# Kernel optimization log

Measured on AMD Instinct MI355X. Metric: run time of the kernel, lower is better.

## Reference

```python
import jax, jax.numpy as jnp
import numpy as np

T = 8192
D_IN = 512
D_QK = 64
D_V = 64


def setup_inputs() -> dict:
    key = jax.random.key(0)
    kx, kq, kk, kv, kl = jax.random.split(key, 5)
    x = jax.random.normal(kx, (T, D_IN), dtype=jnp.float32)
    Wq = jax.random.normal(kq, (D_IN, D_QK), dtype=jnp.float32) * 0.02
    Wk = jax.random.normal(kk, (D_IN, D_QK), dtype=jnp.float32) * 0.02
    Wv = jax.random.normal(kv, (D_IN, D_V), dtype=jnp.float32) * 0.02
    l = jax.random.normal(kl, (T, T), dtype=jnp.float32) * 0.02
    return {"x": x, "Wq": Wq, "Wk": Wk, "Wv": Wv, "l": l}


def reference(x, Wq, Wk, Wv, l):
    # q: [T, d_qk], k: [T, d_qk], v: [T, d_v]
    q = x @ Wq
    k = x @ Wk
    v = x @ Wv
    # scores: [T, S] = (q k^T) elementwise-weighted by learned tril matrix
    scores = jnp.einsum("tn,sn->ts", q, k) * jnp.tril(l)
    # output: [T, d_v]
    return scores @ v
```

## Files before the change

kernel.cpp:

```cpp
#include <hip/hip_runtime.h>
#include <hip/hip_bf16.h>

#define TT 8192
#define DIN 512
#define DQK 64

typedef __attribute__((ext_vector_type(8))) short short8;
typedef __attribute__((ext_vector_type(4))) float f32x4;

__global__ __launch_bounds__(256) void zero_kernel(float* __restrict__ out, int n4)
{
    int i = blockIdx.x * 256 + threadIdx.x;
    if (i < n4) ((f32x4*)out)[i] = (f32x4){0.f, 0.f, 0.f, 0.f};
}

#define PP 72

__global__ __launch_bounds__(256) void proj_kernel(
    const float* __restrict__ x,
    const float* __restrict__ Wq, const float* __restrict__ Wk, const float* __restrict__ Wv,
    __hip_bfloat16* __restrict__ qb, __hip_bfloat16* __restrict__ kb,
    __hip_bfloat16* __restrict__ vt)
{
    __shared__ short xb[64][PP];
    __shared__ short wb[3][64][PP];

    const int rowBase = blockIdx.x * 64;
    const int tid = threadIdx.x;
    const int lane = tid & 63;
    const int w = tid >> 6;
    const int lo = lane & 15, hi = lane >> 4;

    f32x4 acc[3][4];
    #pragma unroll
    for (int m = 0; m < 3; ++m)
        #pragma unroll
        for (int cf = 0; cf < 4; ++cf) acc[m][cf] = (f32x4){0.f, 0.f, 0.f, 0.f};

    for (int kk = 0; kk < DIN; kk += 64) {
        {
            const int r = tid >> 2;
            const int c0 = (tid & 3) * 16;
            const float* xp = x + (size_t)(rowBase + r) * DIN + kk + c0;
            short tmp[16];
            #pragma unroll
            for (int j = 0; j < 16; ++j) {
                __hip_bfloat16 h = __float2bfloat16(xp[j]);
                tmp[j] = *(short*)&h;
            }
            *(short8*)&xb[r][c0]     = *(short8*)&tmp[0];
            *(short8*)&xb[r][c0 + 8] = *(short8*)&tmp[8];
        }
        {
            const int kr = tid >> 2;
            const int c0 = (tid & 3) * 16;
            #pragma unroll
            for (int m = 0; m < 3; ++m) {
                const float* Wm = (m == 0 ? Wq : (m == 1 ? Wk : Wv));
                const float* wp = Wm + (size_t)(kk + kr) * DQK + c0;
                #pragma unroll
                for (int j = 0; j < 16; ++j) {
                    __hip_bfloat16 h = __float2bfloat16(wp[j]);
                    wb[m][c0 + j][kr] = *(short*)&h;
                }
            }
        }
        __syncthreads();

        short8 a0 = *(short8*)&xb[w * 16 + lo][hi * 8];
        short8 a1 = *(short8*)&xb[w * 16 + lo][32 + hi * 8];
        #pragma unroll
        for (int m = 0; m < 3; ++m) {
            #pragma unroll
            for (int cf = 0; cf < 4; ++cf) {
                short8 b0 = *(short8*)&wb[m][cf * 16 + lo][hi * 8];
                short8 b1 = *(short8*)&wb[m][cf * 16 + lo][32 + hi * 8];
                acc[m][cf] = __builtin_amdgcn_mfma_f32_16x16x32_bf16(a0, b0, acc[m][cf], 0, 0, 0);
                acc[m][cf] = __builtin_amdgcn_mfma_f32_16x16x32_bf16(a1, b1, acc[m][cf], 0, 0, 0);
            }
        }
        __syncthreads();
    }

    #pragma unroll
    for (int cf = 0; cf < 4; ++cf) {
        #pragma unroll
        for (int r = 0; r < 4; ++r) {
            const int tg = rowBase + w * 16 + hi * 4 + r;
            const int d  = cf * 16 + lo;
            __hip_bfloat16 hq = __float2bfloat16(acc[0][cf][r]);
            __hip_bfloat16 hk = __float2bfloat16(acc[1][cf][r]);
            __hip_bfloat16 hv = __float2bfloat16(acc[2][cf][r]);
            qb[(size_t)tg * DQK + d] = hq;
            kb[(size_t)tg * DQK + d] = hk;
            vt[(size_t)d * TT + tg]  = hv;
        }
    }
}

#define TM 128
#define TS 64
#define SCHUNK 256
#define LP 72

__global__ __launch_bounds__(512) void attn_kernel(
    const __hip_bfloat16* __restrict__ qb,
    const __hip_bfloat16* __restrict__ kb,
    const __hip_bfloat16* __restrict__ vt,
    const float* __restrict__ l,
    float* __restrict__ out)
{
    __shared__ short K_lds[TS][LP];
    __shared__ short V_lds[DQK][LP];
    __shared__ short S_lds[8][16][LP];

    const int t0 = blockIdx.x * TM;
    const int sStart = blockIdx.y * SCHUNK;
    if (sStart >= t0 + TM) return;
    const int sEnd = min(sStart + SCHUNK, t0 + TM);

    const int tid = threadIdx.x;
    const int lane = tid & 63;
    const int w = tid >> 6;
    const int lo = lane & 15, hi = lane >> 4;
    const int trow = t0 + w * 16;

    short8 qf0, qf1;
    {
        const short* qp = (const short*)qb + (size_t)(trow + lo) * DQK;
        qf0 = *(const short8*)(qp + hi * 8);
        qf1 = *(const short8*)(qp + 32 + hi * 8);
    }

    f32x4 acc_o[4];
    #pragma unroll
    for (int i = 0; i < 4; ++i) acc_o[i] = (f32x4){0.f, 0.f, 0.f, 0.f};

    for (int s0 = sStart; s0 < sEnd; s0 += TS) {
        {
            const int row = tid >> 3;
            const int c8 = (tid & 7) * 8;
            *(short8*)&K_lds[row][c8] =
                *(const short8*)((const short*)kb + (size_t)(s0 + row) * DQK + c8);
            *(short8*)&V_lds[row][c8] =
                *(const short8*)((const short*)vt + (size_t)row * TT + s0 + c8);
        }
        __syncthreads();

        const bool active = (s0 <= trow + 15);

        if (active) {
            float lv[4][4];
            #pragma unroll
            for (int sub = 0; sub < 4; ++sub) {
                const int s_glob = s0 + sub * 16 + lo;
                #pragma unroll
                for (int r = 0; r < 4; ++r) {
                    const int tg = trow + hi * 4 + r;
                    lv[sub][r] = (s_glob <= tg) ? l[(size_t)tg * TT + s_glob] : 0.f;
                }
            }
            #pragma unroll
            for (int sub = 0; sub < 4; ++sub) {
                f32x4 acc = (f32x4){0.f, 0.f, 0.f, 0.f};
                short8 b0 = *(short8*)&K_lds[sub * 16 + lo][hi * 8];
                short8 b1 = *(short8*)&K_lds[sub * 16 + lo][32 + hi * 8];
                acc = __builtin_amdgcn_mfma_f32_16x16x32_bf16(qf0, b0, acc, 0, 0, 0);
                acc = __builtin_amdgcn_mfma_f32_16x16x32_bf16(qf1, b1, acc, 0, 0, 0);
                #pragma unroll
                for (int r = 0; r < 4; ++r) {
                    float sv = acc[r] * lv[sub][r];
                    __hip_bfloat16 h = __float2bfloat16(sv);
                    S_lds[w][hi * 4 + r][sub * 16 + lo] = *(short*)&h;
                }
            }
        }
        __syncthreads();

        if (active) {
            short8 a0 = *(short8*)&S_lds[w][lo][hi * 8];
            short8 a1 = *(short8*)&S_lds[w][lo][32 + hi * 8];
            #pragma unroll
            for (int ds = 0; ds < 4; ++ds) {
                short8 b0 = *(short8*)&V_lds[ds * 16 + lo][hi * 8];
                short8 b1 = *(short8*)&V_lds[ds * 16 + lo][32 + hi * 8];
                acc_o[ds] = __builtin_amdgcn_mfma_f32_16x16x32_bf16(a0, b0, acc_o[ds], 0, 0, 0);
                acc_o[ds] = __builtin_amdgcn_mfma_f32_16x16x32_bf16(a1, b1, acc_o[ds], 0, 0, 0);
            }
        }
        __syncthreads();
    }

    #pragma unroll
    for (int ds = 0; ds < 4; ++ds) {
        #pragma unroll
        for (int r = 0; r < 4; ++r) {
            const int tg = trow + hi * 4 + r;
            atomicAdd(&out[(size_t)tg * DQK + ds * 16 + lo], acc_o[ds][r]);
        }
    }
}

extern "C" void kernel_launch(void* const* d_in, const int* in_sizes, int n_in,
                              void* d_out, int out_size, void* d_ws, size_t ws_size,
                              hipStream_t stream) {
    const float* x  = (const float*)d_in[0];
    const float* Wq = (const float*)d_in[1];
    const float* Wk = (const float*)d_in[2];
    const float* Wv = (const float*)d_in[3];
    const float* l  = (const float*)d_in[4];
    float* out = (float*)d_out;

    __hip_bfloat16* qb = (__hip_bfloat16*)d_ws;
    __hip_bfloat16* kb = qb + (size_t)TT * DQK;
    __hip_bfloat16* vt = kb + (size_t)TT * DQK;

    zero_kernel<<<(out_size / 4 + 255) / 256, 256, 0, stream>>>(out, out_size / 4);
    proj_kernel<<<TT / 64, 256, 0, stream>>>(x, Wq, Wk, Wv, qb, kb, vt);
    attn_kernel<<<dim3(TT / TM, TT / SCHUNK), 512, 0, stream>>>(qb, kb, vt, l, out);
}
```

Measured before the change: 77.82 us.

## Prefetch next l tile in registers, pre-convert weights, vectorize x loads

```diff
diff --git a/kernel.cpp b/kernel.cpp
--- a/kernel.cpp
+++ b/kernel.cpp
@@ -14,11 +14,47 @@
     if (i < n4) ((f32x4*)out)[i] = (f32x4){0.f, 0.f, 0.f, 0.f};
 }
 
+__global__ __launch_bounds__(256) void wconv_kernel(
+    const float* __restrict__ Wq, const float* __restrict__ Wk, const float* __restrict__ Wv,
+    __hip_bfloat16* __restrict__ wtb)
+{
+    __shared__ float tile[64][65];
+    const int m = blockIdx.y;
+    const float* W = m == 0 ? Wq : (m == 1 ? Wk : Wv);
+    const int k0 = blockIdx.x * 64;
+    const int tid = threadIdx.x;
+
+    {
+        const int col4 = (tid & 15) * 4;
+        #pragma unroll
+        for (int it = 0; it < 4; ++it) {
+            const int row = (tid >> 4) + it * 16;
+            float4 v = *(const float4*)&W[(size_t)(k0 + row) * DQK + col4];
+            tile[row][col4 + 0] = v.x; tile[row][col4 + 1] = v.y;
+            tile[row][col4 + 2] = v.z; tile[row][col4 + 3] = v.w;
+        }
+    }
+    __syncthreads();
+    {
+        const int d = tid >> 2;
+        const int kc = (tid & 3) * 16;
+        short tmp[16];
+        #pragma unroll
+        for (int j = 0; j < 16; ++j) {
+            __hip_bfloat16 h = __float2bfloat16(tile[kc + j][d]);
+            tmp[j] = *(short*)&h;
+        }
+        short* dst = (short*)wtb + ((size_t)m * 64 + d) * DIN + k0 + kc;
+        *(short8*)dst       = *(short8*)&tmp[0];
+        *(short8*)(dst + 8) = *(short8*)&tmp[8];
+    }
+}
+
 #define PP 72
 
 __global__ __launch_bounds__(256) void proj_kernel(
     const float* __restrict__ x,
-    const float* __restrict__ Wq, const float* __restrict__ Wk, const float* __restrict__ Wv,
+    const __hip_bfloat16* __restrict__ wtb,
     __hip_bfloat16* __restrict__ qb, __hip_bfloat16* __restrict__ kb,
     __hip_bfloat16* __restrict__ vt)
 {
@@ -44,25 +80,26 @@
             const float* xp = x + (size_t)(rowBase + r) * DIN + kk + c0;
             short tmp[16];
             #pragma unroll
-            for (int j = 0; j < 16; ++j) {
-                __hip_bfloat16 h = __float2bfloat16(xp[j]);
-                tmp[j] = *(short*)&h;
+            for (int j = 0; j < 16; j += 4) {
+                float4 v = *(const float4*)(xp + j);
+                __hip_bfloat16 h0 = __float2bfloat16(v.x);
+                __hip_bfloat16 h1 = __float2bfloat16(v.y);
+                __hip_bfloat16 h2 = __float2bfloat16(v.z);
+                __hip_bfloat16 h3 = __float2bfloat16(v.w);
+                tmp[j + 0] = *(short*)&h0; tmp[j + 1] = *(short*)&h1;
+                tmp[j + 2] = *(short*)&h2; tmp[j + 3] = *(short*)&h3;
             }
             *(short8*)&xb[r][c0]     = *(short8*)&tmp[0];
             *(short8*)&xb[r][c0 + 8] = *(short8*)&tmp[8];
         }
         {
-            const int kr = tid >> 2;
-            const int c0 = (tid & 3) * 16;
+            const int d = tid >> 2;
+            const int kc = (tid & 3) * 16;
             #pragma unroll
             for (int m = 0; m < 3; ++m) {
-                const float* Wm = (m == 0 ? Wq : (m == 1 ? Wk : Wv));
-                const float* wp = Wm + (size_t)(kk + kr) * DQK + c0;
-                #pragma unroll
-                for (int j = 0; j < 16; ++j) {
-                    __hip_bfloat16 h = __float2bfloat16(wp[j]);
-                    wb[m][c0 + j][kr] = *(short*)&h;
-                }
+                const short* src = (const short*)wtb + ((size_t)m * 64 + d) * DIN + kk + kc;
+                *(short8*)&wb[m][d][kc]     = *(const short8*)src;
+                *(short8*)&wb[m][d][kc + 8] = *(const short8*)(src + 8);
             }
         }
         __syncthreads();
@@ -136,6 +173,20 @@
     #pragma unroll
     for (int i = 0; i < 4; ++i) acc_o[i] = (f32x4){0.f, 0.f, 0.f, 0.f};
 
+    float lvC[4][4];
+    float lvN[4][4] = {{0.f}};
+    {
+        #pragma unroll
+        for (int sub = 0; sub < 4; ++sub) {
+            const int s_glob = sStart + sub * 16 + lo;
+            #pragma unroll
+            for (int r = 0; r < 4; ++r) {
+                const int tg = trow + hi * 4 + r;
+                lvC[sub][r] = (s_glob <= tg) ? l[(size_t)tg * TT + s_glob] : 0.f;
+            }
+        }
+    }
+
     for (int s0 = sStart; s0 < sEnd; s0 += TS) {
         {
             const int row = tid >> 3;
@@ -148,18 +199,22 @@
         __syncthreads();
 
         const bool active = (s0 <= trow + 15);
-
-        if (active) {
-            float lv[4][4];
+        const int sN = s0 + TS;
+        const bool act_next = (sN < sEnd) && (sN <= trow + 15);
+
+        if (act_next) {
             #pragma unroll
             for (int sub = 0; sub < 4; ++sub) {
-                const int s_glob = s0 + sub * 16 + lo;
+                const int s_glob = sN + sub * 16 + lo;
                 #pragma unroll
                 for (int r = 0; r < 4; ++r) {
                     const int tg = trow + hi * 4 + r;
-                    lv[sub][r] = (s_glob <= tg) ? l[(size_t)tg * TT + s_glob] : 0.f;
+                    lvN[sub][r] = (s_glob <= tg) ? l[(size_t)tg * TT + s_glob] : 0.f;
                 }
             }
+        }
+
+        if (active) {
             #pragma unroll
             for (int sub = 0; sub < 4; ++sub) {
                 f32x4 acc = (f32x4){0.f, 0.f, 0.f, 0.f};
@@ -169,15 +224,11 @@
                 acc = __builtin_amdgcn_mfma_f32_16x16x32_bf16(qf1, b1, acc, 0, 0, 0);
                 #pragma unroll
                 for (int r = 0; r < 4; ++r) {
-                    float sv = acc[r] * lv[sub][r];
+                    float sv = acc[r] * lvC[sub][r];
                     __hip_bfloat16 h = __float2bfloat16(sv);
                     S_lds[w][hi * 4 + r][sub * 16 + lo] = *(short*)&h;
                 }
             }
-        }
-        __syncthreads();
-
-        if (active) {
             short8 a0 = *(short8*)&S_lds[w][lo][hi * 8];
             short8 a1 = *(short8*)&S_lds[w][lo][32 + hi * 8];
             #pragma unroll
@@ -189,6 +240,12 @@
             }
         }
         __syncthreads();
+
+        #pragma unroll
+        for (int sub = 0; sub < 4; ++sub)
+            #pragma unroll
+            for (int r = 0; r < 4; ++r)
+                lvC[sub][r] = lvN[sub][r];
     }
 
     #pragma unroll
@@ -211,11 +268,13 @@
     const float* l  = (const float*)d_in[4];
     float* out = (float*)d_out;
 
-    __hip_bfloat16* qb = (__hip_bfloat16*)d_ws;
-    __hip_bfloat16* kb = qb + (size_t)TT * DQK;
-    __hip_bfloat16* vt = kb + (size_t)TT * DQK;
+    __hip_bfloat16* qb  = (__hip_bfloat16*)d_ws;
+    __hip_bfloat16* kb  = qb + (size_t)TT * DQK;
+    __hip_bfloat16* vt  = kb + (size_t)TT * DQK;
+    __hip_bfloat16* wtb = vt + (size_t)TT * DQK;
 
     zero_kernel<<<(out_size / 4 + 255) / 256, 256, 0, stream>>>(out, out_size / 4);
-    proj_kernel<<<TT / 64, 256, 0, stream>>>(x, Wq, Wk, Wv, qb, kb, vt);
+    wconv_kernel<<<dim3(DIN / 64, 3), 256, 0, stream>>>(Wq, Wk, Wv, wtb);
+    proj_kernel<<<TT / 64, 256, 0, stream>>>(x, wtb, qb, kb, vt);
     attn_kernel<<<dim3(TT / TM, TT / SCHUNK), 512, 0, stream>>>(qb, kb, vt, l, out);
 }
```

Result: faster. 72.57 us (-6.7%).
